# Kernel tuning notes

Hardware: AMD Instinct MI355X
Metric: run time of the kernel (lower is better)

## Reference

```python
import jax, jax.numpy as jnp
import numpy as np

N_NODES = 21
LN_EPS = 1e-5


def setup_inputs() -> dict:
    key = jax.random.key(0)
    ks = jax.random.split(key, 10)
    B, d, gh, E = 8192, 256, 512, 40
    h = jax.random.normal(ks[0], (B, N_NODES, d), dtype=jnp.float32)
    src_index = jax.random.randint(ks[1], (E,), 0, N_NODES)
    dst_index = jax.random.randint(ks[2], (E,), 0, N_NODES)
    # LayerNorm params
    ln_w = jnp.ones((d,), jnp.float32)
    ln_b = jnp.zeros((d,), jnp.float32)
    # value_proj: Linear(d, d), stored as (in, out)
    Wv = jax.random.normal(ks[3], (d, d), dtype=jnp.float32) / np.sqrt(d)
    bv = jax.random.normal(ks[4], (d,), dtype=jnp.float32) * 0.01
    # gate_mlp: Linear(2d, gh) -> GELU -> Linear(gh, 1)
    W1 = jax.random.normal(ks[5], (2 * d, gh), dtype=jnp.float32) / np.sqrt(2 * d)
    b1 = jax.random.normal(ks[6], (gh,), dtype=jnp.float32) * 0.01
    W2 = jax.random.normal(ks[7], (gh, 1), dtype=jnp.float32) / np.sqrt(gh)
    b2 = jax.random.normal(ks[8], (1,), dtype=jnp.float32) * 0.01
    return {"h": h, "src_index": src_index, "dst_index": dst_index,
            "ln_w": ln_w, "ln_b": ln_b, "Wv": Wv, "bv": bv,
            "W1": W1, "b1": b1, "W2": W2, "b2": b2}


def _layernorm(x, w, b):
    mu = jnp.mean(x, axis=-1, keepdims=True)
    var = jnp.mean(jnp.square(x - mu), axis=-1, keepdims=True)
    return (x - mu) * jax.lax.rsqrt(var + LN_EPS) * w + b


def reference(h, src_index, dst_index, ln_w, ln_b, Wv, bv, W1, b1, W2, b2):
    residual = h
    x = _layernorm(h, ln_w, ln_b)                      # (B, 21, d)
    src_feat = x[:, src_index, :]                      # (B, E, d) gather
    dst_feat = x[:, dst_index, :]                      # (B, E, d) gather
    values = jnp.einsum('bed,df->bef', src_feat, Wv) + bv  # (B, E, d)
    g = jnp.concatenate([src_feat, dst_feat], axis=-1) # (B, E, 2d)
    g = jax.nn.gelu(jnp.einsum('bec,ch->beh', g, W1) + b1, approximate=False)
    gates = jax.nn.sigmoid(jnp.einsum('beh,ho->beo', g, W2) + b2)  # (B, E, 1)
    messages = gates * values                          # (B, E, d)
    aggregated = jnp.zeros_like(x).at[:, dst_index, :].add(messages)  # scatter-add over nodes
    return residual + aggregated
```

## Files before the change

kernel.cpp:

```cpp
#include <hip/hip_runtime.h>
#include <hip/hip_bf16.h>
#include <math.h>

typedef __attribute__((ext_vector_type(8))) short short8;
typedef __attribute__((ext_vector_type(4))) float f32x4;

#define NN    21
#define DD    256
#define GH    512
#define NE    40
#define BT    3
#define MROWS (BT * NN)
#define MPAD  64
#define NTHR  256
#define UVSTR 36

__device__ __forceinline__ f32x4 mfma16(short8 a, short8 b, f32x4 c) {
    return __builtin_amdgcn_mfma_f32_16x16x32_bf16(a, b, c, 0, 0, 0);
}

__global__ void prep_weights(const float* __restrict__ Wv, const float* __restrict__ W1,
                             __hip_bfloat16* __restrict__ WvT,
                             __hip_bfloat16* __restrict__ WtT,
                             __hip_bfloat16* __restrict__ WbT) {
    __shared__ float tile[64][65];
    int bi = blockIdx.x;
    const float* src;
    int ld, tc, th;
    bool isW1 = bi < 64;
    if (isW1) { src = W1; ld = 512; tc = (bi & 7) * 64; th = (bi >> 3) * 64; }
    else      { int b = bi - 64; src = Wv; ld = 256; tc = (b & 3) * 64; th = (b >> 2) * 64; }
    for (int i = 0; i < 16; ++i) {
        int e = threadIdx.x + 256 * i;
        int r = e >> 6, cc = e & 63;
        tile[r][cc] = src[(size_t)(tc + r) * ld + th + cc];
    }
    __syncthreads();
    for (int i = 0; i < 16; ++i) {
        int e  = threadIdx.x + 256 * i;
        int r2 = e >> 6, cc2 = e & 63;
        float v = tile[cc2][r2];
        int hh = th + r2, c = tc + cc2;
        if (isW1) {
            if (c < 256) WtT[hh * 256 + c]         = __float2bfloat16(v);
            else         WbT[hh * 256 + (c - 256)] = __float2bfloat16(v);
        } else {
            WvT[hh * 256 + c] = __float2bfloat16(v);
        }
    }
}

#define GELU_GATE(zu, zv, zb, zw)  do {                              \
    float z_ = (zu) + (zv) + (zb);                                   \
    float y_ = 1.5957691216f * (z_ + 0.044715f * z_ * z_ * z_);      \
    float s_ = 1.0f / (1.0f + __expf(-y_));                          \
    gacc += z_ * s_ * (zw); } while (0)

__launch_bounds__(NTHR, 4)
__global__ void fused_kernel(const float* __restrict__ hin,
                             const int* __restrict__ srci, const int* __restrict__ dsti,
                             const float* __restrict__ lnw, const float* __restrict__ lnb,
                             const float* __restrict__ bv,  const float* __restrict__ b1,
                             const float* __restrict__ W2,  const float* __restrict__ b2,
                             const __hip_bfloat16* __restrict__ WvT,
                             const __hip_bfloat16* __restrict__ WtT,
                             const __hip_bfloat16* __restrict__ WbT,
                             float* __restrict__ out, int Btotal) {
    __shared__ __align__(16) char smem[32768];
    __shared__ __align__(16) float b1s[GH], w2s[GH], bvs[DD];
    __shared__ float gates[BT * NE];
    __shared__ int   srcs[NE], dsts[NE];
    __shared__ int   csr_off[NN + 1], csr_cur[NN], csr_eid[NE];

    const int tid  = threadIdx.x;
    const int lane = tid & 63;
    const int w    = tid >> 6;
    const int b0   = blockIdx.x * BT;

    if (tid < NE) { srcs[tid] = srci[tid]; dsts[tid] = dsti[tid]; }
    b1s[tid] = b1[tid];  b1s[tid + 256] = b1[tid + 256];
    w2s[tid] = W2[tid];  w2s[tid + 256] = W2[tid + 256];
    bvs[tid] = bv[tid];
    if (tid <= NN) csr_off[tid] = 0;
    int myd = (tid < NE) ? dsti[tid] : 0;
    __syncthreads();
    if (tid < NE) atomicAdd(&csr_off[myd + 1], 1);

    const int s_row0 = tid >> 5;
    const int s_pg   = tid & 31;
    const int s_cg   = s_pg ^ (s_row0 & 7);
    char* const s_dst = smem + s_row0 * 512 + s_pg * 16;
    const __hip_bfloat16* const s_wt = WtT + (size_t)s_row0 * 256 + s_cg * 8;
    const __hip_bfloat16* const s_wb = WbT + (size_t)s_row0 * 256 + s_cg * 8;
    const __hip_bfloat16* const s_wv = WvT + (size_t)s_row0 * 256 + s_cg * 8;

    {
        float4 wgt = ((const float4*)lnw)[lane];
        float4 bta = ((const float4*)lnb)[lane];
        for (int r = w; r < MPAD; r += 4) {
            int b_loc = r / NN;
            int node  = r - b_loc * NN;
            bool valid = (r < MROWS) && (b0 + b_loc < Btotal);
            float4 h4 = {0.f, 0.f, 0.f, 0.f};
            if (valid)
                h4 = *(const float4*)(hin + ((size_t)(b0 + b_loc) * NN + node) * DD + lane * 4);
            float s  = h4.x + h4.y + h4.z + h4.w;
            float ss = h4.x*h4.x + h4.y*h4.y + h4.z*h4.z + h4.w*h4.w;
            for (int off = 32; off; off >>= 1) {
                s  += __shfl_xor(s,  off);
                ss += __shfl_xor(ss, off);
            }
            float mu   = s * (1.0f / 256.0f);
            float rstd = rsqrtf(ss * (1.0f / 256.0f) - mu * mu + 1e-5f);
            __align__(8) __hip_bfloat16 t[4];
            if (valid) {
                t[0] = __float2bfloat16((h4.x - mu) * rstd * wgt.x + bta.x);
                t[1] = __float2bfloat16((h4.y - mu) * rstd * wgt.y + bta.y);
                t[2] = __float2bfloat16((h4.z - mu) * rstd * wgt.z + bta.z);
                t[3] = __float2bfloat16((h4.w - mu) * rstd * wgt.w + bta.w);
            } else {
                __hip_bfloat16 z = __float2bfloat16(0.0f);
                t[0] = z; t[1] = z; t[2] = z; t[3] = z;
            }
            char* dst = smem + r * 512 + ((((lane >> 1) ^ (r & 7)) << 4) | ((lane & 1) << 3));
            *(ushort4*)dst = *(ushort4*)&t[0];
        }
    }
    __syncthreads();

    if (tid == 0) {
        for (int n = 0; n < NN; ++n) csr_off[n + 1] += csr_off[n];
        for (int n = 0; n < NN; ++n) csr_cur[n] = csr_off[n];
        for (int e = 0; e < NE; ++e) { int d = dsts[e]; csr_eid[csr_cur[d]++] = e; }
    }

    const int mq   = w & 1;
    const int nsel = w >> 1;
    const int l15  = lane & 15;
    const int lq   = lane >> 4;
    short8 afr[2][8];
    #pragma unroll
    for (int mt = 0; mt < 2; ++mt) {
        int r = 32 * mq + 16 * mt + l15;
        const char* rowp = smem + r * 512;
        int swz = r & 7;
        #pragma unroll
        for (int ki = 0; ki < 8; ++ki)
            afr[mt][ki] = *(const short8*)(rowp + ((((ki << 2) + lq) ^ swz) << 4));
    }
    __syncthreads();

    float* uvp = (float*)(smem + 16384);

    const bool gactive = tid < 2 * BT * NE;
    int rs = 0, rd = 0;
    if (gactive) {
        int p  = tid >> 1;
        int pb = p / NE, pe = p - pb * NE;
        rs = pb * NN + srcs[pe];
        rd = pb * NN + dsts[pe];
    }
    const int jh = tid & 1;

    {
        *(float4*)(s_dst         ) = *(const float4*)(s_wt       );
        *(float4*)(s_dst +  4096 ) = *(const float4*)(s_wt + 2048);
        *(float4*)(s_dst +  8192 ) = *(const float4*)(s_wb       );
        *(float4*)(s_dst + 12288 ) = *(const float4*)(s_wb + 2048);
    }
    __syncthreads();

    float gacc = 0.0f;
    const int   brow_r = 16 * nsel + l15;
    const char* browp  = smem + brow_r * 512;
    const int   bswz   = l15 & 7;
    for (int c = 0; c < 32; ++c) {
        float4 stg0, stg1, stg2, stg3;
        if (c + 1 < 32) {
            const __hip_bfloat16* pt = s_wt + (size_t)(c + 1) * 4096;
            const __hip_bfloat16* pb = s_wb + (size_t)(c + 1) * 4096;
            stg0 = *(const float4*)(pt       );
            stg1 = *(const float4*)(pt + 2048);
            stg2 = *(const float4*)(pb       );
            stg3 = *(const float4*)(pb + 2048);
        }
        f32x4 acc0 = {0.f,0.f,0.f,0.f}, acc1 = {0.f,0.f,0.f,0.f};
        #pragma unroll
        for (int ki = 0; ki < 8; ++ki) {
            short8 bf = *(const short8*)(browp + ((((ki << 2) + lq) ^ bswz) << 4));
            acc0 = mfma16(afr[0][ki], bf, acc0);
            acc1 = mfma16(afr[1][ki], bf, acc1);
        }
        #pragma unroll
        for (int r = 0; r < 4; ++r) {
            int col = 16 * nsel + l15;
            uvp[(32 * mq +      4 * lq + r) * UVSTR + col] = acc0[r];
            uvp[(32 * mq + 16 + 4 * lq + r) * UVSTR + col] = acc1[r];
        }
        __syncthreads();
        if (c + 1 < 32) {
            *(float4*)(s_dst        ) = stg0;
            *(float4*)(s_dst +  4096) = stg1;
            *(float4*)(s_dst +  8192) = stg2;
            *(float4*)(s_dst + 12288) = stg3;
        }
        if (gactive) {
            const float4* up4 = (const float4*)(uvp + rs * UVSTR + jh * 8);
            const float4* vp4 = (const float4*)(uvp + rd * UVSTR + 16 + jh * 8);
            const float4* b14 = (const float4*)(b1s + c * 16 + jh * 8);
            const float4* w24 = (const float4*)(w2s + c * 16 + jh * 8);
            float4 ua = up4[0], ub = up4[1];
            float4 va = vp4[0], vb = vp4[1];
            float4 ba = b14[0], bb = b14[1];
            float4 wa = w24[0], wb = w24[1];
            GELU_GATE(ua.x, va.x, ba.x, wa.x);
            GELU_GATE(ua.y, va.y, ba.y, wa.y);
            GELU_GATE(ua.z, va.z, ba.z, wa.z);
            GELU_GATE(ua.w, va.w, ba.w, wa.w);
            GELU_GATE(ub.x, vb.x, bb.x, wb.x);
            GELU_GATE(ub.y, vb.y, bb.y, wb.y);
            GELU_GATE(ub.z, vb.z, bb.z, wb.z);
            GELU_GATE(ub.w, vb.w, bb.w, wb.w);
        }
        __syncthreads();
    }

    if (gactive) {
        float other = __shfl_xor(gacc, 1);
        if (jh == 0) {
            float tot = gacc + other + b2[0];
            gates[tid >> 1] = 1.0f / (1.0f + __expf(-tot));
        }
    }
    {
        *(float4*)(s_dst        ) = *(const float4*)(s_wv       );
        *(float4*)(s_dst +  4096) = *(const float4*)(s_wv + 2048);
        *(float4*)(s_dst +  8192) = *(const float4*)(s_wv + 4096);
        *(float4*)(s_dst + 12288) = *(const float4*)(s_wv + 6144);
    }
    __syncthreads();

    for (int vc = 0; vc < 8; ++vc) {
        float4 stg0, stg1, stg2, stg3;
        if (vc + 1 < 8) {
            const __hip_bfloat16* pv = s_wv + (size_t)(vc + 1) * 8192;
            stg0 = *(const float4*)(pv       );
            stg1 = *(const float4*)(pv + 2048);
            stg2 = *(const float4*)(pv + 4096);
            stg3 = *(const float4*)(pv + 6144);
        }
        f32x4 acc0 = {0.f,0.f,0.f,0.f}, acc1 = {0.f,0.f,0.f,0.f};
        #pragma unroll
        for (int ki = 0; ki < 8; ++ki) {
            short8 bf = *(const short8*)(browp + ((((ki << 2) + lq) ^ bswz) << 4));
            acc0 = mfma16(afr[0][ki], bf, acc0);
            acc1 = mfma16(afr[1][ki], bf, acc1);
        }
        #pragma unroll
        for (int r = 0; r < 4; ++r) {
            int col = 16 * nsel + l15;
            float bvv = bvs[vc * 32 + col];
            uvp[(32 * mq +      4 * lq + r) * UVSTR + col] = acc0[r] + bvv;
            uvp[(32 * mq + 16 + 4 * lq + r) * UVSTR + col] = acc1[r] + bvv;
        }
        __syncthreads();
        if (vc + 1 < 8) {
            *(float4*)(s_dst        ) = stg0;
            *(float4*)(s_dst +  4096) = stg1;
            *(float4*)(s_dst +  8192) = stg2;
            *(float4*)(s_dst + 12288) = stg3;
        }
        for (int q = tid; q < MROWS * 8; q += NTHR) {
            int row = q >> 3, g = q & 7;
            int b_loc = row / NN;
            int node  = row - b_loc * NN;
            if (b0 + b_loc < Btotal) {
                size_t ga = ((size_t)(b0 + b_loc) * NN + node) * DD + vc * 32 + g * 4;
                float4 hv = *(const float4*)(hin + ga);
                float a0 = hv.x, a1 = hv.y, a2 = hv.z, a3 = hv.w;
                int e1 = csr_off[node + 1];
                for (int ii = csr_off[node]; ii < e1; ++ii) {
                    int e  = csr_eid[ii];
                    float gv = gates[b_loc * NE + e];
                    const float* vp = uvp + (b_loc * NN + srcs[e]) * UVSTR + g * 4;
                    a0 += gv * vp[0]; a1 += gv * vp[1];
                    a2 += gv * vp[2]; a3 += gv * vp[3];
                }
                float4 o = {a0, a1, a2, a3};
                *(float4*)(out + ga) = o;
            }
        }
        __syncthreads();
    }
}

extern "C" void kernel_launch(void* const* d_in, const int* in_sizes, int n_in,
                              void* d_out, int out_size, void* d_ws, size_t ws_size,
                              hipStream_t stream) {
    const float* h   = (const float*)d_in[0];
    const int*  srci = (const int*)d_in[1];
    const int*  dsti = (const int*)d_in[2];
    const float* lnw = (const float*)d_in[3];
    const float* lnb = (const float*)d_in[4];
    const float* Wv  = (const float*)d_in[5];
    const float* bv  = (const float*)d_in[6];
    const float* W1  = (const float*)d_in[7];
    const float* b1  = (const float*)d_in[8];
    const float* W2  = (const float*)d_in[9];
    const float* b2  = (const float*)d_in[10];
    float* out = (float*)d_out;

    __hip_bfloat16* WvT = (__hip_bfloat16*)d_ws;
    __hip_bfloat16* WtT = WvT + 256 * 256;
    __hip_bfloat16* WbT = WtT + 512 * 256;

    int Btotal = in_sizes[0] / (NN * DD);
    prep_weights<<<80, 256, 0, stream>>>(Wv, W1, WvT, WtT, WbT);
    int grid = (Btotal + BT - 1) / BT;
    fused_kernel<<<grid, NTHR, 0, stream>>>(h, srci, dsti, lnw, lnb, bv, b1, W2, b2,
                                            WvT, WtT, WbT, out, Btotal);
}
```

Measured before the change: 530.3 us.

## Process eight batches per block with wave-owned A tiles and deeper weight prefetch

Measured after the change: 646.3 us. 1.22x slower.

```diff
diff --git a/kernel.cpp b/kernel.cpp
--- a/kernel.cpp
+++ b/kernel.cpp
@@ -9,15 +9,20 @@
 #define DD    256
 #define GH    512
 #define NE    40
-#define BT    3
+#define BT    8
 #define MROWS (BT * NN)
-#define MPAD  64
+#define MPAD  192
 #define NTHR  256
 #define UVSTR 36
+#define NPAIR (BT * NE)
+#define WST_OFF 36864
 
 __device__ __forceinline__ f32x4 mfma16(short8 a, short8 b, f32x4 c) {
     return __builtin_amdgcn_mfma_f32_16x16x32_bf16(a, b, c, 0, 0, 0);
 }
+
+#define BAR()     asm volatile("s_waitcnt lgkmcnt(0)\n\ts_barrier" ::: "memory")
+#define WAITLDS() asm volatile("s_waitcnt lgkmcnt(0)" ::: "memory")
 
 __global__ void prep_weights(const float* __restrict__ Wv, const float* __restrict__ W1,
                              __hip_bfloat16* __restrict__ WvT,
@@ -50,13 +55,14 @@
     }
 }
 
-#define GELU_GATE(zu, zv, zb, zw)  do {                              \
-    float z_ = (zu) + (zv) + (zb);                                   \
-    float y_ = 1.5957691216f * (z_ + 0.044715f * z_ * z_ * z_);      \
-    float s_ = 1.0f / (1.0f + __expf(-y_));                          \
-    gacc += z_ * s_ * (zw); } while (0)
-
-__launch_bounds__(NTHR, 4)
+#define GG(acc, zu, zv, zb, zw)  do {                                 \
+    float z_ = (zu) + (zv) + (zb);                                    \
+    float t_ = __builtin_fmaf(0.10294480f, z_ * z_, 2.3022081f);      \
+    float e_ = __builtin_amdgcn_exp2f(-(z_ * t_));                    \
+    float s_ = __builtin_amdgcn_rcpf(1.0f + e_);                      \
+    (acc) = __builtin_fmaf(z_ * s_, (zw), (acc)); } while (0)
+
+__launch_bounds__(NTHR, 2)
 __global__ void fused_kernel(const float* __restrict__ hin,
                              const int* __restrict__ srci, const int* __restrict__ dsti,
                              const float* __restrict__ lnw, const float* __restrict__ lnb,
@@ -66,9 +72,9 @@
                              const __hip_bfloat16* __restrict__ WtT,
                              const __hip_bfloat16* __restrict__ WbT,
                              float* __restrict__ out, int Btotal) {
-    __shared__ __align__(16) char smem[32768];
+    __shared__ __align__(16) char smem[53248];
     __shared__ __align__(16) float b1s[GH], w2s[GH], bvs[DD];
-    __shared__ float gates[BT * NE];
+    __shared__ float gates[NPAIR];
     __shared__ int   srcs[NE], dsts[NE];
     __shared__ int   csr_off[NN + 1], csr_cur[NN], csr_eid[NE];
 
@@ -89,44 +95,76 @@
     const int s_row0 = tid >> 5;
     const int s_pg   = tid & 31;
     const int s_cg   = s_pg ^ (s_row0 & 7);
-    char* const s_dst = smem + s_row0 * 512 + s_pg * 16;
+    char* const wstb  = smem + WST_OFF;
+    char* const s_dst = wstb + s_row0 * 512 + s_pg * 16;
     const __hip_bfloat16* const s_wt = WtT + (size_t)s_row0 * 256 + s_cg * 8;
     const __hip_bfloat16* const s_wb = WbT + (size_t)s_row0 * 256 + s_cg * 8;
     const __hip_bfloat16* const s_wv = WvT + (size_t)s_row0 * 256 + s_cg * 8;
 
+    float4 stg0 = *(const float4*)(s_wt);
+    float4 stg1 = *(const float4*)(s_wt + 2048);
+    float4 stg2 = *(const float4*)(s_wb);
+    float4 stg3 = *(const float4*)(s_wb + 2048);
+    const float b2v = b2[0];
+
+    const int l15 = lane & 15;
+    const int lq  = lane >> 4;
+    char* const lnbuf = smem + w * 8192;
+    short8 afr[3][8];
     {
-        float4 wgt = ((const float4*)lnw)[lane];
-        float4 bta = ((const float4*)lnb)[lane];
-        for (int r = w; r < MPAD; r += 4) {
-            int b_loc = r / NN;
-            int node  = r - b_loc * NN;
-            bool valid = (r < MROWS) && (b0 + b_loc < Btotal);
-            float4 h4 = {0.f, 0.f, 0.f, 0.f};
-            if (valid)
-                h4 = *(const float4*)(hin + ((size_t)(b0 + b_loc) * NN + node) * DD + lane * 4);
-            float s  = h4.x + h4.y + h4.z + h4.w;
-            float ss = h4.x*h4.x + h4.y*h4.y + h4.z*h4.z + h4.w*h4.w;
-            for (int off = 32; off; off >>= 1) {
-                s  += __shfl_xor(s,  off);
-                ss += __shfl_xor(ss, off);
-            }
-            float mu   = s * (1.0f / 256.0f);
-            float rstd = rsqrtf(ss * (1.0f / 256.0f) - mu * mu + 1e-5f);
-            __align__(8) __hip_bfloat16 t[4];
-            if (valid) {
-                t[0] = __float2bfloat16((h4.x - mu) * rstd * wgt.x + bta.x);
-                t[1] = __float2bfloat16((h4.y - mu) * rstd * wgt.y + bta.y);
-                t[2] = __float2bfloat16((h4.z - mu) * rstd * wgt.z + bta.z);
-                t[3] = __float2bfloat16((h4.w - mu) * rstd * wgt.w + bta.w);
-            } else {
-                __hip_bfloat16 z = __float2bfloat16(0.0f);
-                t[0] = z; t[1] = z; t[2] = z; t[3] = z;
-            }
-            char* dst = smem + r * 512 + ((((lane >> 1) ^ (r & 7)) << 4) | ((lane & 1) << 3));
-            *(ushort4*)dst = *(ushort4*)&t[0];
-        }
-    }
-    __syncthreads();
+        const float4 wgt = ((const float4*)lnw)[lane];
+        const float4 bta = ((const float4*)lnb)[lane];
+        #pragma unroll 1
+        for (int mt = 0; mt < 3; ++mt) {
+            #pragma unroll 4
+            for (int rr = 0; rr < 16; ++rr) {
+                const int r     = 48 * w + 16 * mt + rr;
+                const int b_loc = r / NN;
+                const int node  = r - b_loc * NN;
+                const bool valid = (r < MROWS) && (b0 + b_loc < Btotal);
+                float4 h4 = {0.f, 0.f, 0.f, 0.f};
+                if (valid)
+                    h4 = *(const float4*)(hin + ((size_t)(b0 + b_loc) * NN + node) * DD + lane * 4);
+                float s  = h4.x + h4.y + h4.z + h4.w;
+                float ss = h4.x*h4.x + h4.y*h4.y + h4.z*h4.z + h4.w*h4.w;
+                for (int off = 32; off; off >>= 1) {
+                    s  += __shfl_xor(s,  off);
+                    ss += __shfl_xor(ss, off);
+                }
+                float mu   = s * (1.0f / 256.0f);
+                float rstd = rsqrtf(ss * (1.0f / 256.0f) - mu * mu + 1e-5f);
+                __align__(8) __hip_bfloat16 t[4];
+                if (valid) {
+                    t[0] = __float2bfloat16((h4.x - mu) * rstd * wgt.x + bta.x);
+                    t[1] = __float2bfloat16((h4.y - mu) * rstd * wgt.y + bta.y);
+                    t[2] = __float2bfloat16((h4.z - mu) * rstd * wgt.z + bta.z);
+                    t[3] = __float2bfloat16((h4.w - mu) * rstd * wgt.w + bta.w);
+                } else {
+                    __hip_bfloat16 z = __float2bfloat16(0.0f);
+                    t[0] = z; t[1] = z; t[2] = z; t[3] = z;
+                }
+                char* dst = lnbuf + rr * 512 +
+                            ((((lane >> 1) ^ (rr & 7)) << 4) | ((lane & 1) << 3));
+                *(ushort4*)dst = *(ushort4*)&t[0];
+            }
+            WAITLDS();
+            #pragma unroll
+            for (int ki = 0; ki < 8; ++ki)
+                afr[mt][ki] = *(const short8*)(lnbuf + l15 * 512 +
+                                  ((((ki << 2) + lq) ^ (l15 & 7)) << 4));
+            WAITLDS();
+        }
+    }
+
+    *(float4*)(s_dst        ) = stg0;
+    *(float4*)(s_dst +  4096) = stg1;
+    *(float4*)(s_dst +  8192) = stg2;
+    *(float4*)(s_dst + 12288) = stg3;
+    stg0 = *(const float4*)(s_wt + 4096);
+    stg1 = *(const float4*)(s_wt + 4096 + 2048);
+    stg2 = *(const float4*)(s_wb + 4096);
+    stg3 = *(const float4*)(s_wb + 4096 + 2048);
+    BAR();
 
     if (tid == 0) {
         for (int n = 0; n < NN; ++n) csr_off[n + 1] += csr_off[n];
@@ -134,141 +172,159 @@
         for (int e = 0; e < NE; ++e) { int d = dsts[e]; csr_eid[csr_cur[d]++] = e; }
     }
 
-    const int mq   = w & 1;
-    const int nsel = w >> 1;
-    const int l15  = lane & 15;
-    const int lq   = lane >> 4;
-    short8 afr[2][8];
-    #pragma unroll
-    for (int mt = 0; mt < 2; ++mt) {
-        int r = 32 * mq + 16 * mt + l15;
-        const char* rowp = smem + r * 512;
-        int swz = r & 7;
-        #pragma unroll
-        for (int ki = 0; ki < 8; ++ki)
-            afr[mt][ki] = *(const short8*)(rowp + ((((ki << 2) + lq) ^ swz) << 4));
-    }
-    __syncthreads();
-
-    float* uvp = (float*)(smem + 16384);
-
-    const bool gactive = tid < 2 * BT * NE;
-    int rs = 0, rd = 0;
-    if (gactive) {
-        int p  = tid >> 1;
-        int pb = p / NE, pe = p - pb * NE;
-        rs = pb * NN + srcs[pe];
-        rd = pb * NN + dsts[pe];
-    }
-    const int jh = tid & 1;
-
-    {
-        *(float4*)(s_dst         ) = *(const float4*)(s_wt       );
-        *(float4*)(s_dst +  4096 ) = *(const float4*)(s_wt + 2048);
-        *(float4*)(s_dst +  8192 ) = *(const float4*)(s_wb       );
-        *(float4*)(s_dst + 12288 ) = *(const float4*)(s_wb + 2048);
-    }
-    __syncthreads();
-
-    float gacc = 0.0f;
-    const int   brow_r = 16 * nsel + l15;
-    const char* browp  = smem + brow_r * 512;
-    const int   bswz   = l15 & 7;
+    float* const uvp = (float*)smem;
+
+    const bool gact = tid < NPAIR / 2;
+    int rs0 = 0, rd0 = 0, rs1 = 0, rd1 = 0;
+    if (gact) {
+        int p0 = 2 * tid,  p1 = 2 * tid + 1;
+        int pb0 = p0 / NE, pe0 = p0 - pb0 * NE;
+        int pb1 = p1 / NE, pe1 = p1 - pb1 * NE;
+        rs0 = pb0 * NN + srcs[pe0];  rd0 = pb0 * NN + dsts[pe0];
+        rs1 = pb1 * NN + srcs[pe1];  rd1 = pb1 * NN + dsts[pe1];
+    }
+
+    const char* const bU = wstb + l15 * 512;
+    const char* const bV = wstb + (16 + l15) * 512;
+    const int bswz  = l15 & 7;
+    const int rbase = 48 * w + 4 * lq;
+
+    float gacc0 = 0.0f, gacc1 = 0.0f;
+
+    #pragma unroll 1
     for (int c = 0; c < 32; ++c) {
-        float4 stg0, stg1, stg2, stg3;
-        if (c + 1 < 32) {
-            const __hip_bfloat16* pt = s_wt + (size_t)(c + 1) * 4096;
-            const __hip_bfloat16* pb = s_wb + (size_t)(c + 1) * 4096;
-            stg0 = *(const float4*)(pt       );
-            stg1 = *(const float4*)(pt + 2048);
-            stg2 = *(const float4*)(pb       );
-            stg3 = *(const float4*)(pb + 2048);
-        }
-        f32x4 acc0 = {0.f,0.f,0.f,0.f}, acc1 = {0.f,0.f,0.f,0.f};
+        f32x4 aU0 = {0.f,0.f,0.f,0.f}, aU1 = {0.f,0.f,0.f,0.f}, aU2 = {0.f,0.f,0.f,0.f};
+        f32x4 aV0 = {0.f,0.f,0.f,0.f}, aV1 = {0.f,0.f,0.f,0.f}, aV2 = {0.f,0.f,0.f,0.f};
         #pragma unroll
         for (int ki = 0; ki < 8; ++ki) {
-            short8 bf = *(const short8*)(browp + ((((ki << 2) + lq) ^ bswz) << 4));
-            acc0 = mfma16(afr[0][ki], bf, acc0);
-            acc1 = mfma16(afr[1][ki], bf, acc1);
+            const int off = (((ki << 2) + lq) ^ bswz) << 4;
+            short8 bu = *(const short8*)(bU + off);
+            short8 bw = *(const short8*)(bV + off);
+            aU0 = mfma16(afr[0][ki], bu, aU0);
+            aU1 = mfma16(afr[1][ki], bu, aU1);
+            aU2 = mfma16(afr[2][ki], bu, aU2);
+            aV0 = mfma16(afr[0][ki], bw, aV0);
+            aV1 = mfma16(afr[1][ki], bw, aV1);
+            aV2 = mfma16(afr[2][ki], bw, aV2);
         }
         #pragma unroll
         for (int r = 0; r < 4; ++r) {
-            int col = 16 * nsel + l15;
-            uvp[(32 * mq +      4 * lq + r) * UVSTR + col] = acc0[r];
-            uvp[(32 * mq + 16 + 4 * lq + r) * UVSTR + col] = acc1[r];
-        }
-        __syncthreads();
+            uvp[(rbase      + r) * UVSTR      + l15] = aU0[r];
+            uvp[(rbase      + r) * UVSTR + 16 + l15] = aV0[r];
+            uvp[(rbase + 16 + r) * UVSTR      + l15] = aU1[r];
+            uvp[(rbase + 16 + r) * UVSTR + 16 + l15] = aV1[r];
+            uvp[(rbase + 32 + r) * UVSTR      + l15] = aU2[r];
+            uvp[(rbase + 32 + r) * UVSTR + 16 + l15] = aV2[r];
+        }
+        BAR();
         if (c + 1 < 32) {
             *(float4*)(s_dst        ) = stg0;
             *(float4*)(s_dst +  4096) = stg1;
             *(float4*)(s_dst +  8192) = stg2;
             *(float4*)(s_dst + 12288) = stg3;
-        }
-        if (gactive) {
-            const float4* up4 = (const float4*)(uvp + rs * UVSTR + jh * 8);
-            const float4* vp4 = (const float4*)(uvp + rd * UVSTR + 16 + jh * 8);
-            const float4* b14 = (const float4*)(b1s + c * 16 + jh * 8);
-            const float4* w24 = (const float4*)(w2s + c * 16 + jh * 8);
-            float4 ua = up4[0], ub = up4[1];
-            float4 va = vp4[0], vb = vp4[1];
-            float4 ba = b14[0], bb = b14[1];
-            float4 wa = w24[0], wb = w24[1];
-            GELU_GATE(ua.x, va.x, ba.x, wa.x);
-            GELU_GATE(ua.y, va.y, ba.y, wa.y);
-            GELU_GATE(ua.z, va.z, ba.z, wa.z);
-            GELU_GATE(ua.w, va.w, ba.w, wa.w);
-            GELU_GATE(ub.x, vb.x, bb.x, wb.x);
-            GELU_GATE(ub.y, vb.y, bb.y, wb.y);
-            GELU_GATE(ub.z, vb.z, bb.z, wb.z);
-            GELU_GATE(ub.w, vb.w, bb.w, wb.w);
-        }
-        __syncthreads();
-    }
-
-    if (gactive) {
-        float other = __shfl_xor(gacc, 1);
-        if (jh == 0) {
-            float tot = gacc + other + b2[0];
-            gates[tid >> 1] = 1.0f / (1.0f + __expf(-tot));
-        }
-    }
-    {
-        *(float4*)(s_dst        ) = *(const float4*)(s_wv       );
-        *(float4*)(s_dst +  4096) = *(const float4*)(s_wv + 2048);
-        *(float4*)(s_dst +  8192) = *(const float4*)(s_wv + 4096);
-        *(float4*)(s_dst + 12288) = *(const float4*)(s_wv + 6144);
-    }
-    __syncthreads();
-
+            if (c + 2 < 32) {
+                const __hip_bfloat16* pt = s_wt + (size_t)(c + 2) * 4096;
+                const __hip_bfloat16* pb = s_wb + (size_t)(c + 2) * 4096;
+                stg0 = *(const float4*)(pt);
+                stg1 = *(const float4*)(pt + 2048);
+                stg2 = *(const float4*)(pb);
+                stg3 = *(const float4*)(pb + 2048);
+            } else {
+                stg0 = *(const float4*)(s_wv);
+                stg1 = *(const float4*)(s_wv + 2048);
+                stg2 = *(const float4*)(s_wv + 4096);
+                stg3 = *(const float4*)(s_wv + 6144);
+            }
+        }
+        if (gact) {
+            const float4* bb = (const float4*)(b1s + c * 16);
+            const float4* ww = (const float4*)(w2s + c * 16);
+            {
+                const float4* u = (const float4*)(uvp + rs0 * UVSTR);
+                const float4* v = (const float4*)(uvp + rd0 * UVSTR + 16);
+                #pragma unroll
+                for (int q = 0; q < 4; ++q) {
+                    float4 ua = u[q], va = v[q], b4 = bb[q], w4 = ww[q];
+                    GG(gacc0, ua.x, va.x, b4.x, w4.x);
+                    GG(gacc0, ua.y, va.y, b4.y, w4.y);
+                    GG(gacc0, ua.z, va.z, b4.z, w4.z);
+                    GG(gacc0, ua.w, va.w, b4.w, w4.w);
+                }
+            }
+            {
+                const float4* u = (const float4*)(uvp + rs1 * UVSTR);
+                const float4* v = (const float4*)(uvp + rd1 * UVSTR + 16);
+                #pragma unroll
+                for (int q = 0; q < 4; ++q) {
+                    float4 ua = u[q], va = v[q], b4 = bb[q], w4 = ww[q];
+                    GG(gacc1, ua.x, va.x, b4.x, w4.x);
+                    GG(gacc1, ua.y, va.y, b4.y, w4.y);
+                    GG(gacc1, ua.z, va.z, b4.z, w4.z);
+                    GG(gacc1, ua.w, va.w, b4.w, w4.w);
+                }
+            }
+        }
+        BAR();
+    }
+
+    if (gact) {
+        float e0 = __builtin_amdgcn_exp2f(-1.442695041f * (gacc0 + b2v));
+        float e1 = __builtin_amdgcn_exp2f(-1.442695041f * (gacc1 + b2v));
+        gates[2 * tid]     = __builtin_amdgcn_rcpf(1.0f + e0);
+        gates[2 * tid + 1] = __builtin_amdgcn_rcpf(1.0f + e1);
+    }
+    *(float4*)(s_dst        ) = stg0;
+    *(float4*)(s_dst +  4096) = stg1;
+    *(float4*)(s_dst +  8192) = stg2;
+    *(float4*)(s_dst + 12288) = stg3;
+    stg0 = *(const float4*)(s_wv + 8192);
+    stg1 = *(const float4*)(s_wv + 8192 + 2048);
+    stg2 = *(const float4*)(s_wv + 8192 + 4096);
+    stg3 = *(const float4*)(s_wv + 8192 + 6144);
+    BAR();
+
+    #pragma unroll 1
     for (int vc = 0; vc < 8; ++vc) {
-        float4 stg0, stg1, stg2, stg3;
-        if (vc + 1 < 8) {
-            const __hip_bfloat16* pv = s_wv + (size_t)(vc + 1) * 8192;
-            stg0 = *(const float4*)(pv       );
-            stg1 = *(const float4*)(pv + 2048);
-            stg2 = *(const float4*)(pv + 4096);
-            stg3 = *(const float4*)(pv + 6144);
-        }
-        f32x4 acc0 = {0.f,0.f,0.f,0.f}, acc1 = {0.f,0.f,0.f,0.f};
+        f32x4 pA0 = {0.f,0.f,0.f,0.f}, pA1 = {0.f,0.f,0.f,0.f}, pA2 = {0.f,0.f,0.f,0.f};
+        f32x4 pB0 = {0.f,0.f,0.f,0.f}, pB1 = {0.f,0.f,0.f,0.f}, pB2 = {0.f,0.f,0.f,0.f};
         #pragma unroll
         for (int ki = 0; ki < 8; ++ki) {
-            short8 bf = *(const short8*)(browp + ((((ki << 2) + lq) ^ bswz) << 4));
-            acc0 = mfma16(afr[0][ki], bf, acc0);
-            acc1 = mfma16(afr[1][ki], bf, acc1);
-        }
-        #pragma unroll
-        for (int r = 0; r < 4; ++r) {
-            int col = 16 * nsel + l15;
-            float bvv = bvs[vc * 32 + col];
-            uvp[(32 * mq +      4 * lq + r) * UVSTR + col] = acc0[r] + bvv;
-            uvp[(32 * mq + 16 + 4 * lq + r) * UVSTR + col] = acc1[r] + bvv;
-        }
-        __syncthreads();
+            const int off = (((ki << 2) + lq) ^ bswz) << 4;
+            short8 bu = *(const short8*)(bU + off);
+            short8 bw = *(const short8*)(bV + off);
+            pA0 = mfma16(afr[0][ki], bu, pA0);
+            pA1 = mfma16(afr[1][ki], bu, pA1);
+            pA2 = mfma16(afr[2][ki], bu, pA2);
+            pB0 = mfma16(afr[0][ki], bw, pB0);
+            pB1 = mfma16(afr[1][ki], bw, pB1);
+            pB2 = mfma16(afr[2][ki], bw, pB2);
+        }
+        {
+            const float bv0 = bvs[vc * 32 + l15];
+            const float bv1 = bvs[vc * 32 + 16 + l15];
+            #pragma unroll
+            for (int r = 0; r < 4; ++r) {
+                uvp[(rbase      + r) * UVSTR      + l15] = pA0[r] + bv0;
+                uvp[(rbase      + r) * UVSTR + 16 + l15] = pB0[r] + bv1;
+                uvp[(rbase + 16 + r) * UVSTR      + l15] = pA1[r] + bv0;
+                uvp[(rbase + 16 + r) * UVSTR + 16 + l15] = pB1[r] + bv1;
+                uvp[(rbase + 32 + r) * UVSTR      + l15] = pA2[r] + bv0;
+                uvp[(rbase + 32 + r) * UVSTR + 16 + l15] = pB2[r] + bv1;
+            }
+        }
+        BAR();
         if (vc + 1 < 8) {
             *(float4*)(s_dst        ) = stg0;
             *(float4*)(s_dst +  4096) = stg1;
             *(float4*)(s_dst +  8192) = stg2;
             *(float4*)(s_dst + 12288) = stg3;
+            if (vc + 2 < 8) {
+                const __hip_bfloat16* pv = s_wv + (size_t)(vc + 2) * 8192;
+                stg0 = *(const float4*)(pv);
+                stg1 = *(const float4*)(pv + 2048);
+                stg2 = *(const float4*)(pv + 4096);
+                stg3 = *(const float4*)(pv + 6144);
+            }
         }
         for (int q = tid; q < MROWS * 8; q += NTHR) {
             int row = q >> 3, g = q & 7;
@@ -290,7 +346,7 @@
                 *(float4*)(out + ga) = o;
             }
         }
-        __syncthreads();
+        BAR();
     }
 }
 
```
